# Kernel tuning notes

Measured on AMD Instinct MI355X. Metric: run time of the kernel, lower is better.

## Reference

```python
import jax, jax.numpy as jnp
import numpy as np

L = 32            # fixed label space replacing torch.unique (labels in [0, L))
DELTA_AGG = 0.5
DELTA_DIS = 1.5
REG_W = 0.001


def safe_norm(sq):
    # sqrt with zero-safe gradient: returns 0 where sq == 0
    safe = jnp.where(sq > 0, sq, 1.0)
    return jnp.where(sq > 0, jnp.sqrt(safe), 0.0)


def _single(emb, instance, kernel, training_mask):
    D = emb.shape[0]
    tm = training_mask > 0.5
    kn = kernel > 0.5
    inst = jnp.where(tm, instance, 0).reshape(-1)          # (N,) masked instance labels
    inst_k = jnp.where(tm & kn, instance, 0).reshape(-1)   # (N,) kernel-region labels
    embf = emb.reshape(D, -1).T                            # (N, D)
    ones = jnp.ones(inst.shape, dtype=jnp.float32)

    # per-label kernel means (emb_mean), label 0 stays zero as in torch
    cnt_k = jax.ops.segment_sum(ones, inst_k, num_segments=L)            # (L,)
    sum_k = jax.ops.segment_sum(embf, inst_k, num_segments=L)            # (L, D)
    emb_mean = sum_k / jnp.maximum(cnt_k, 1.0)[:, None]
    emb_mean = emb_mean.at[0].set(0.0)

    present = cnt_k > 0
    num_instance = jnp.sum(present.astype(jnp.int32))
    nz = present & (jnp.arange(L) > 0)

    # aggregation loss: per-pixel distance to own instance's kernel mean
    diff = embf - emb_mean[inst]                                          # (N, D)
    dist = safe_norm(jnp.sum(diff * diff, axis=1))
    val = jnp.log(jax.nn.relu(dist - DELTA_AGG) ** 2 + 1.0)
    sum_v = jax.ops.segment_sum(val, inst, num_segments=L)
    cnt = jax.ops.segment_sum(ones, inst, num_segments=L)
    l_agg_per = sum_v / jnp.maximum(cnt, 1.0)
    l_agg = jnp.sum(jnp.where(nz, l_agg_per, 0.0)) / jnp.maximum(num_instance - 1, 1)

    # discrimination loss: all pairs of distinct non-background present labels
    pdiff = emb_mean[:, None, :] - emb_mean[None, :, :]                   # (L, L, D)
    pdist = safe_norm(jnp.sum(pdiff * pdiff, axis=-1))
    pval = jnp.log(jax.nn.relu(2.0 * DELTA_DIS - pdist) ** 2 + 1.0)
    pmask = nz[:, None] & nz[None, :] & ~jnp.eye(L, dtype=bool)
    n_pairs = jnp.sum(pmask.astype(jnp.float32))
    l_dis = jnp.sum(jnp.where(pmask, pval, 0.0)) / jnp.maximum(n_pairs, 1.0)
    l_dis = jnp.where(num_instance > 2, l_dis, 0.0)

    # regularizer over the num_instance present columns of emb_mean
    reg = jnp.log(safe_norm(jnp.sum(emb_mean * emb_mean, axis=1)) + 1.0)
    l_reg = jnp.sum(jnp.where(present, reg, 0.0)) / jnp.maximum(num_instance, 1) * REG_W

    loss = l_agg + l_dis + l_reg
    return jnp.where(num_instance <= 1, 0.0, loss)


def setup_inputs() -> dict:
    key = jax.random.key(0)
    k1, k2, k3, k4 = jax.random.split(key, 4)
    B, D, H, W = 8, 4, 736, 736
    emb = jax.random.normal(k1, (B, D, H, W), dtype=jnp.float32)
    instance = jax.random.randint(k2, (B, H, W), 0, L, dtype=jnp.int32)
    kernel = jax.random.uniform(k3, (B, H, W), dtype=jnp.float32)
    training_mask = jax.random.uniform(k4, (B, H, W), dtype=jnp.float32)
    return {"emb": emb, "instance": instance, "kernel": kernel, "training_mask": training_mask}


def reference(emb, instance, kernel, training_mask):
    return jax.vmap(_single)(emb, instance, kernel, training_mask)
```

## Files before the change

### kernel.cpp

```cpp
#include <hip/hip_runtime.h>

#define LBL 32
#define NPIX (736 * 736)
#define NQ (NPIX / 4)
#define QPB 512
#define NBA 265
#define BATCH 8
#define DELTA_AGG 0.5f
#define DELTA_DIS 1.5f
#define REG_W 0.001f

#define CE_BASE 0
#define LAB_BASE (BATCH * NPIX * 2)
#define PA_BASE (LAB_BASE + BATCH * NQ)
#define RED_BASE (PA_BASE + BATCH * NBA * 192)
#define PC_BASE (RED_BASE + BATCH * 256)

__device__ __forceinline__ unsigned short f2bf(float f) {
  unsigned int u = __float_as_uint(f);
  unsigned int r = u + 0x7FFFu + ((u >> 16) & 1u);
  return (unsigned short)(r >> 16);
}
__device__ __forceinline__ float bfl(unsigned int w) {
  return __uint_as_float(w << 16);
}
__device__ __forceinline__ float bfh(unsigned int w) {
  return __uint_as_float(w & 0xFFFF0000u);
}

__global__ __launch_bounds__(256) void kA(
    const float* __restrict__ emb, const int* __restrict__ inst,
    const float* __restrict__ kern, const float* __restrict__ mask,
    float* __restrict__ ws) {
  const int b = blockIdx.y;
  const int t = threadIdx.x;
  __shared__ float s_cnt[LBL];
  __shared__ float s_sum[LBL * 4];
  __shared__ float s_cta[LBL];
  if (t < LBL) { s_cnt[t] = 0.f; s_cta[t] = 0.f; }
  if (t < LBL * 4) s_sum[t] = 0.f;
  __syncthreads();

  const long base = (long)b * NPIX;
  const float* ebase = emb + (long)b * 4 * NPIX;
  const int4* ip = (const int4*)(inst + base);
  const float4* kp = (const float4*)(kern + base);
  const float4* mp = (const float4*)(mask + base);
  const float4* p0 = (const float4*)(ebase);
  const float4* p1 = (const float4*)(ebase + NPIX);
  const float4* p2 = (const float4*)(ebase + 2 * NPIX);
  const float4* p3 = (const float4*)(ebase + 3 * NPIX);

  const int q0 = blockIdx.x * QPB + t;
  const int q1 = q0 + 256;
  const bool v1 = (q1 < NQ);

  const int4 iva = ip[q0];
  const float4 kva = kp[q0], mva = mp[q0];
  const float4 ea0 = p0[q0], ea1 = p1[q0], ea2 = p2[q0], ea3 = p3[q0];
  int4 ivb;
  float4 kvb, mvb, fb0, fb1, fb2, fb3;
  if (v1) {
    ivb = ip[q1]; kvb = kp[q1]; mvb = mp[q1];
    fb0 = p0[q1]; fb1 = p1[q1]; fb2 = p2[q1]; fb3 = p3[q1];
  }

  bool has0 = false;
  unsigned int* labp = (unsigned int*)(ws + LAB_BASE) + (size_t)b * NQ;
  uint4* cep = (uint4*)(ws + CE_BASE) + (size_t)b * NQ * 2;

  {
    const int labs[4] = {iva.x, iva.y, iva.z, iva.w};
    const float ks[4] = {kva.x, kva.y, kva.z, kva.w};
    const float ms[4] = {mva.x, mva.y, mva.z, mva.w};
    const float c0[4] = {ea0.x, ea0.y, ea0.z, ea0.w};
    const float c1[4] = {ea1.x, ea1.y, ea1.z, ea1.w};
    const float c2[4] = {ea2.x, ea2.y, ea2.z, ea2.w};
    const float c3[4] = {ea3.x, ea3.y, ea3.z, ea3.w};
    unsigned int labw = 0;
    union { unsigned short us[16]; uint4 v[2]; } pk;
#pragma unroll
    for (int j = 0; j < 4; j++) {
      const bool m = ms[j] > 0.5f;
      const int li = m ? labs[j] : 0;
      const int lk = (m && ks[j] > 0.5f) ? labs[j] : 0;
      labw |= ((unsigned int)li) << (8 * j);
      pk.us[j * 4 + 0] = f2bf(c0[j]);
      pk.us[j * 4 + 1] = f2bf(c1[j]);
      pk.us[j * 4 + 2] = f2bf(c2[j]);
      pk.us[j * 4 + 3] = f2bf(c3[j]);
      if (li > 0) atomicAdd(&s_cta[li], 1.0f);
      if (lk > 0) {
        atomicAdd(&s_cnt[lk], 1.0f);
        atomicAdd(&s_sum[lk * 4 + 0], c0[j]);
        atomicAdd(&s_sum[lk * 4 + 1], c1[j]);
        atomicAdd(&s_sum[lk * 4 + 2], c2[j]);
        atomicAdd(&s_sum[lk * 4 + 3], c3[j]);
      } else {
        has0 = true;
      }
    }
    labp[q0] = labw;
    cep[(size_t)q0 * 2] = pk.v[0];
    cep[(size_t)q0 * 2 + 1] = pk.v[1];
  }
  if (v1) {
    const int labs[4] = {ivb.x, ivb.y, ivb.z, ivb.w};
    const float ks[4] = {kvb.x, kvb.y, kvb.z, kvb.w};
    const float ms[4] = {mvb.x, mvb.y, mvb.z, mvb.w};
    const float c0[4] = {fb0.x, fb0.y, fb0.z, fb0.w};
    const float c1[4] = {fb1.x, fb1.y, fb1.z, fb1.w};
    const float c2[4] = {fb2.x, fb2.y, fb2.z, fb2.w};
    const float c3[4] = {fb3.x, fb3.y, fb3.z, fb3.w};
    unsigned int labw = 0;
    union { unsigned short us[16]; uint4 v[2]; } pk;
#pragma unroll
    for (int j = 0; j < 4; j++) {
      const bool m = ms[j] > 0.5f;
      const int li = m ? labs[j] : 0;
      const int lk = (m && ks[j] > 0.5f) ? labs[j] : 0;
      labw |= ((unsigned int)li) << (8 * j);
      pk.us[j * 4 + 0] = f2bf(c0[j]);
      pk.us[j * 4 + 1] = f2bf(c1[j]);
      pk.us[j * 4 + 2] = f2bf(c2[j]);
      pk.us[j * 4 + 3] = f2bf(c3[j]);
      if (li > 0) atomicAdd(&s_cta[li], 1.0f);
      if (lk > 0) {
        atomicAdd(&s_cnt[lk], 1.0f);
        atomicAdd(&s_sum[lk * 4 + 0], c0[j]);
        atomicAdd(&s_sum[lk * 4 + 1], c1[j]);
        atomicAdd(&s_sum[lk * 4 + 2], c2[j]);
        atomicAdd(&s_sum[lk * 4 + 3], c3[j]);
      } else {
        has0 = true;
      }
    }
    labp[q1] = labw;
    cep[(size_t)q1 * 2] = pk.v[0];
    cep[(size_t)q1 * 2 + 1] = pk.v[1];
  }

  if (has0) s_cnt[0] = 1.0f;
  __syncthreads();
  float* po = ws + PA_BASE + ((size_t)b * NBA + blockIdx.x) * 192;
  if (t < 192)
    po[t] = (t < 32) ? s_cnt[t] : (t < 160 ? s_sum[t - 32] : s_cta[t - 160]);
}

__global__ __launch_bounds__(256) void kB(float* __restrict__ ws) {
  const int b = blockIdx.y;
  const int col = blockIdx.x * 4 + (threadIdx.x >> 6);
  const int lane = threadIdx.x & 63;
  const float* pa = ws + PA_BASE + (size_t)b * NBA * 192 + col;
  float s = 0.f;
  for (int g = lane; g < NBA; g += 64) s += pa[(size_t)g * 192];
#pragma unroll
  for (int o = 32; o > 0; o >>= 1) s += __shfl_down(s, o);
  if (lane == 0) ws[RED_BASE + b * 256 + col] = s;
}

__global__ __launch_bounds__(256) void kC(float* __restrict__ ws) {
  const int b = blockIdx.y;
  const int t = threadIdx.x;
  __shared__ float s_mean[LBL * 4];
  __shared__ float s_val[LBL];
  const float* rd = ws + RED_BASE + b * 256;
  if (t < LBL * 4) {
    const int l = t >> 2;
    s_mean[t] = (l == 0) ? 0.f : rd[32 + t] / fmaxf(rd[l], 1.0f);
  }
  if (t < LBL) s_val[t] = 0.f;
  __syncthreads();

  const unsigned int* labp = (const unsigned int*)(ws + LAB_BASE) + (size_t)b * NQ;
  const uint4* cep = (const uint4*)(ws + CE_BASE) + (size_t)b * NQ * 2;
  const int q0 = blockIdx.x * QPB + t;
  const int q1 = q0 + 256;
  const bool v1 = (q1 < NQ);

  const unsigned int lwa = labp[q0];
  const uint4 ra0 = cep[(size_t)q0 * 2], ra1 = cep[(size_t)q0 * 2 + 1];
  unsigned int lwb = 0;
  uint4 rb0, rb1;
  if (v1) {
    lwb = labp[q1];
    rb0 = cep[(size_t)q1 * 2];
    rb1 = cep[(size_t)q1 * 2 + 1];
  }

  {
    const unsigned int wlo[4] = {ra0.x, ra0.z, ra1.x, ra1.z};
    const unsigned int whi[4] = {ra0.y, ra0.w, ra1.y, ra1.w};
#pragma unroll
    for (int j = 0; j < 4; j++) {
      const int li = (lwa >> (8 * j)) & 0xFF;
      if (li > 0) {
        const float d0 = bfl(wlo[j]) - s_mean[li * 4 + 0];
        const float d1 = bfh(wlo[j]) - s_mean[li * 4 + 1];
        const float d2 = bfl(whi[j]) - s_mean[li * 4 + 2];
        const float d3 = bfh(whi[j]) - s_mean[li * 4 + 3];
        const float sq = d0 * d0 + d1 * d1 + d2 * d2 + d3 * d3;
        const float dist = (sq > 0.f) ? sqrtf(sq) : 0.f;
        const float tt = fmaxf(dist - DELTA_AGG, 0.f);
        atomicAdd(&s_val[li], logf(fmaf(tt, tt, 1.0f)));
      }
    }
  }
  if (v1) {
    const unsigned int wlo[4] = {rb0.x, rb0.z, rb1.x, rb1.z};
    const unsigned int whi[4] = {rb0.y, rb0.w, rb1.y, rb1.w};
#pragma unroll
    for (int j = 0; j < 4; j++) {
      const int li = (lwb >> (8 * j)) & 0xFF;
      if (li > 0) {
        const float d0 = bfl(wlo[j]) - s_mean[li * 4 + 0];
        const float d1 = bfh(wlo[j]) - s_mean[li * 4 + 1];
        const float d2 = bfl(whi[j]) - s_mean[li * 4 + 2];
        const float d3 = bfh(whi[j]) - s_mean[li * 4 + 3];
        const float sq = d0 * d0 + d1 * d1 + d2 * d2 + d3 * d3;
        const float dist = (sq > 0.f) ? sqrtf(sq) : 0.f;
        const float tt = fmaxf(dist - DELTA_AGG, 0.f);
        atomicAdd(&s_val[li], logf(fmaf(tt, tt, 1.0f)));
      }
    }
  }
  __syncthreads();
  float* po = ws + PC_BASE + ((size_t)b * NBA + blockIdx.x) * 32;
  if (t < 32) po[t] = s_val[t];
}

__global__ __launch_bounds__(1024) void kD(const float* __restrict__ ws,
                                           float* __restrict__ out) {
  const int b = blockIdx.x;
  const int t = threadIdx.x;
  const int col = t >> 5, sub = t & 31;
  const float* pc = ws + PC_BASE + (size_t)b * NBA * 32 + col;
  float s = 0.f;
  for (int g = sub; g < NBA; g += 32) s += pc[(size_t)g * 32];
  __shared__ float red[LBL][33];
  red[col][sub] = s;

  const float* rd = ws + RED_BASE + b * 256;
  __shared__ float sm[LBL * 4];
  __shared__ float scc[LBL];
  __shared__ float sca[LBL];
  if (t >= 512 && t < 640) {
    const int e = t - 512, l = e >> 2;
    sm[e] = (l == 0) ? 0.f : rd[32 + e] / fmaxf(rd[l], 1.0f);
  } else if (t >= 640 && t < 672) {
    scc[t - 640] = rd[t - 640];
  } else if (t >= 672 && t < 704) {
    sca[t - 672] = rd[160 + (t - 672)];
  }
  __syncthreads();
  __shared__ float sv[LBL];
  if (t < 32) {
    float v = 0.f;
#pragma unroll
    for (int k = 0; k < 32; k++) v += red[t][k];
    sv[t] = v;
  }
  __syncthreads();

  if (t < 64) {
    const int lane = t;
    const bool pres = (lane < LBL) && (scc[lane & 31] > 0.f);
    const unsigned long long bal_p = __ballot(pres);
    const int num_instance = __popcll(bal_p);
    const bool nz = pres && (lane > 0);
    const unsigned long long bal_nz = __ballot(nz);

    float agg = 0.f;
    if (nz) agg = sv[lane] / fmaxf(sca[lane], 1.0f);

    float reg = 0.f;
    if (pres) {
      float sq = 0.f;
#pragma unroll
      for (int d = 0; d < 4; d++) sq += sm[lane * 4 + d] * sm[lane * 4 + d];
      const float nrm = (sq > 0.f) ? sqrtf(sq) : 0.f;
      reg = logf(nrm + 1.0f);
    }

    float dis = 0.f, npair = 0.f;
    for (int pi = lane; pi < LBL * LBL; pi += 64) {
      const int i = pi >> 5, j = pi & 31;
      if (i != j && ((bal_nz >> i) & 1ull) && ((bal_nz >> j) & 1ull)) {
        float sq = 0.f;
#pragma unroll
        for (int d = 0; d < 4; d++) {
          const float df = sm[i * 4 + d] - sm[j * 4 + d];
          sq += df * df;
        }
        const float pdist = (sq > 0.f) ? sqrtf(sq) : 0.f;
        const float tt = fmaxf(2.0f * DELTA_DIS - pdist, 0.f);
        dis += logf(fmaf(tt, tt, 1.0f));
        npair += 1.0f;
      }
    }

#pragma unroll
    for (int o = 32; o > 0; o >>= 1) {
      agg += __shfl_down(agg, o);
      reg += __shfl_down(reg, o);
      dis += __shfl_down(dis, o);
      npair += __shfl_down(npair, o);
    }

    if (lane == 0) {
      const float l_agg = agg / fmaxf((float)(num_instance - 1), 1.0f);
      const float l_dis = (num_instance > 2) ? dis / fmaxf(npair, 1.0f) : 0.f;
      const float l_reg = reg / fmaxf((float)num_instance, 1.0f) * REG_W;
      const float loss = l_agg + l_dis + l_reg;
      out[b] = (num_instance <= 1) ? 0.f : loss;
    }
  }
}

extern "C" void kernel_launch(void* const* d_in, const int* in_sizes, int n_in,
                              void* d_out, int out_size, void* d_ws,
                              size_t ws_size, hipStream_t stream) {
  const float* emb = (const float*)d_in[0];
  const int* instance = (const int*)d_in[1];
  const float* kern = (const float*)d_in[2];
  const float* mask = (const float*)d_in[3];
  float* out = (float*)d_out;
  float* ws = (float*)d_ws;

  dim3 gridA(NBA, BATCH);
  kA<<<gridA, 256, 0, stream>>>(emb, instance, kern, mask, ws);
  dim3 gridB(48, BATCH);
  kB<<<gridB, 256, 0, stream>>>(ws);
  kC<<<gridA, 256, 0, stream>>>(ws);
  kD<<<BATCH, 1024, 0, stream>>>(ws, out);
}
```

Measured before the change: 182.8 us.

## Drop bf16 embedding copy, reread fp32 emb in kC, wave-aggregate count atomics

Kernel A no longer writes a packed bf16 copy of the embeddings to the workspace. Kernel C now rereads the original fp32 embeddings instead, which removes a 34MB write and the rounding step at the cost of a larger read in kC (68MB instead of 34MB). Kernel A also groups lanes by label through ballots so that count atomics are issued once per label group per wavefront. This adds ballot overhead, while the per-pixel sum atomics stay unchanged. It also makes kC numerically exact, since it now uses fp32 values rather than bf16.

```diff
diff --git a/kernel.cpp b/kernel.cpp
--- a/kernel.cpp
+++ b/kernel.cpp
@@ -10,22 +10,57 @@
 #define DELTA_DIS 1.5f
 #define REG_W 0.001f
 
-#define CE_BASE 0
-#define LAB_BASE (BATCH * NPIX * 2)
-#define PA_BASE (LAB_BASE + BATCH * NQ)
+#define LAB_BASE 0
+#define PA_BASE (BATCH * NQ)
 #define RED_BASE (PA_BASE + BATCH * NBA * 192)
 #define PC_BASE (RED_BASE + BATCH * 256)
 
-__device__ __forceinline__ unsigned short f2bf(float f) {
-  unsigned int u = __float_as_uint(f);
-  unsigned int r = u + 0x7FFFu + ((u >> 16) & 1u);
-  return (unsigned short)(r >> 16);
-}
-__device__ __forceinline__ float bfl(unsigned int w) {
-  return __uint_as_float(w << 16);
-}
-__device__ __forceinline__ float bfh(unsigned int w) {
-  return __uint_as_float(w & 0xFFFF0000u);
+__device__ __forceinline__ unsigned int procQuad(
+    const int4 iv, const float4 kv, const float4 mv,
+    const float4 e0, const float4 e1, const float4 e2, const float4 e3,
+    const int lane, float* __restrict__ s_cnt, float* __restrict__ s_sum,
+    float* __restrict__ s_cta, bool& has0) {
+  const int labs[4] = {iv.x, iv.y, iv.z, iv.w};
+  const float ks[4] = {kv.x, kv.y, kv.z, kv.w};
+  const float ms[4] = {mv.x, mv.y, mv.z, mv.w};
+  const float c0[4] = {e0.x, e0.y, e0.z, e0.w};
+  const float c1[4] = {e1.x, e1.y, e1.z, e1.w};
+  const float c2[4] = {e2.x, e2.y, e2.z, e2.w};
+  const float c3[4] = {e3.x, e3.y, e3.z, e3.w};
+  unsigned int labw = 0;
+#pragma unroll
+  for (int j = 0; j < 4; j++) {
+    const bool m = ms[j] > 0.5f;
+    const int li = m ? labs[j] : 0;
+    const bool kf = m && (ks[j] > 0.5f);
+    labw |= ((unsigned int)li) << (8 * j);
+    const bool act = li > 0;
+    unsigned long long grp = __ballot(act);
+    const unsigned long long kbal = __ballot(act && kf);
+#pragma unroll
+    for (int bb = 0; bb < 5; bb++) {
+      const unsigned long long bal = __ballot((li >> bb) & 1);
+      grp &= ((li >> bb) & 1) ? bal : ~bal;
+    }
+    if (act) {
+      if ((int)__builtin_ctzll(grp) == lane)
+        atomicAdd(&s_cta[li], (float)__popcll(grp));
+      if (kf) {
+        const unsigned long long gk = grp & kbal;
+        if ((int)__builtin_ctzll(gk) == lane)
+          atomicAdd(&s_cnt[li], (float)__popcll(gk));
+        atomicAdd(&s_sum[li * 4 + 0], c0[j]);
+        atomicAdd(&s_sum[li * 4 + 1], c1[j]);
+        atomicAdd(&s_sum[li * 4 + 2], c2[j]);
+        atomicAdd(&s_sum[li * 4 + 3], c3[j]);
+      } else {
+        has0 = true;
+      }
+    } else {
+      has0 = true;
+    }
+  }
+  return labw;
 }
 
 __global__ __launch_bounds__(256) void kA(
@@ -34,6 +69,7 @@
     float* __restrict__ ws) {
   const int b = blockIdx.y;
   const int t = threadIdx.x;
+  const int lane = t & 63;
   __shared__ float s_cnt[LBL];
   __shared__ float s_sum[LBL * 4];
   __shared__ float s_cta[LBL];
@@ -67,77 +103,12 @@
 
   bool has0 = false;
   unsigned int* labp = (unsigned int*)(ws + LAB_BASE) + (size_t)b * NQ;
-  uint4* cep = (uint4*)(ws + CE_BASE) + (size_t)b * NQ * 2;
-
-  {
-    const int labs[4] = {iva.x, iva.y, iva.z, iva.w};
-    const float ks[4] = {kva.x, kva.y, kva.z, kva.w};
-    const float ms[4] = {mva.x, mva.y, mva.z, mva.w};
-    const float c0[4] = {ea0.x, ea0.y, ea0.z, ea0.w};
-    const float c1[4] = {ea1.x, ea1.y, ea1.z, ea1.w};
-    const float c2[4] = {ea2.x, ea2.y, ea2.z, ea2.w};
-    const float c3[4] = {ea3.x, ea3.y, ea3.z, ea3.w};
-    unsigned int labw = 0;
-    union { unsigned short us[16]; uint4 v[2]; } pk;
-#pragma unroll
-    for (int j = 0; j < 4; j++) {
-      const bool m = ms[j] > 0.5f;
-      const int li = m ? labs[j] : 0;
-      const int lk = (m && ks[j] > 0.5f) ? labs[j] : 0;
-      labw |= ((unsigned int)li) << (8 * j);
-      pk.us[j * 4 + 0] = f2bf(c0[j]);
-      pk.us[j * 4 + 1] = f2bf(c1[j]);
-      pk.us[j * 4 + 2] = f2bf(c2[j]);
-      pk.us[j * 4 + 3] = f2bf(c3[j]);
-      if (li > 0) atomicAdd(&s_cta[li], 1.0f);
-      if (lk > 0) {
-        atomicAdd(&s_cnt[lk], 1.0f);
-        atomicAdd(&s_sum[lk * 4 + 0], c0[j]);
-        atomicAdd(&s_sum[lk * 4 + 1], c1[j]);
-        atomicAdd(&s_sum[lk * 4 + 2], c2[j]);
-        atomicAdd(&s_sum[lk * 4 + 3], c3[j]);
-      } else {
-        has0 = true;
-      }
-    }
-    labp[q0] = labw;
-    cep[(size_t)q0 * 2] = pk.v[0];
-    cep[(size_t)q0 * 2 + 1] = pk.v[1];
-  }
+
+  labp[q0] = procQuad(iva, kva, mva, ea0, ea1, ea2, ea3, lane,
+                      s_cnt, s_sum, s_cta, has0);
   if (v1) {
-    const int labs[4] = {ivb.x, ivb.y, ivb.z, ivb.w};
-    const float ks[4] = {kvb.x, kvb.y, kvb.z, kvb.w};
-    const float ms[4] = {mvb.x, mvb.y, mvb.z, mvb.w};
-    const float c0[4] = {fb0.x, fb0.y, fb0.z, fb0.w};
-    const float c1[4] = {fb1.x, fb1.y, fb1.z, fb1.w};
-    const float c2[4] = {fb2.x, fb2.y, fb2.z, fb2.w};
-    const float c3[4] = {fb3.x, fb3.y, fb3.z, fb3.w};
-    unsigned int labw = 0;
-    union { unsigned short us[16]; uint4 v[2]; } pk;
-#pragma unroll
-    for (int j = 0; j < 4; j++) {
-      const bool m = ms[j] > 0.5f;
-      const int li = m ? labs[j] : 0;
-      const int lk = (m && ks[j] > 0.5f) ? labs[j] : 0;
-      labw |= ((unsigned int)li) << (8 * j);
-      pk.us[j * 4 + 0] = f2bf(c0[j]);
-      pk.us[j * 4 + 1] = f2bf(c1[j]);
-      pk.us[j * 4 + 2] = f2bf(c2[j]);
-      pk.us[j * 4 + 3] = f2bf(c3[j]);
-      if (li > 0) atomicAdd(&s_cta[li], 1.0f);
-      if (lk > 0) {
-        atomicAdd(&s_cnt[lk], 1.0f);
-        atomicAdd(&s_sum[lk * 4 + 0], c0[j]);
-        atomicAdd(&s_sum[lk * 4 + 1], c1[j]);
-        atomicAdd(&s_sum[lk * 4 + 2], c2[j]);
-        atomicAdd(&s_sum[lk * 4 + 3], c3[j]);
-      } else {
-        has0 = true;
-      }
-    }
-    labp[q1] = labw;
-    cep[(size_t)q1 * 2] = pk.v[0];
-    cep[(size_t)q1 * 2 + 1] = pk.v[1];
+    labp[q1] = procQuad(ivb, kvb, mvb, fb0, fb1, fb2, fb3, lane,
+                        s_cnt, s_sum, s_cta, has0);
   }
 
   if (has0) s_cnt[0] = 1.0f;
@@ -159,7 +130,31 @@
   if (lane == 0) ws[RED_BASE + b * 256 + col] = s;
 }
 
-__global__ __launch_bounds__(256) void kC(float* __restrict__ ws) {
+__device__ __forceinline__ void aggQuad(const unsigned int lw,
+    const float4 e0, const float4 e1, const float4 e2, const float4 e3,
+    const float* __restrict__ s_mean, float* __restrict__ s_val) {
+  const float c0[4] = {e0.x, e0.y, e0.z, e0.w};
+  const float c1[4] = {e1.x, e1.y, e1.z, e1.w};
+  const float c2[4] = {e2.x, e2.y, e2.z, e2.w};
+  const float c3[4] = {e3.x, e3.y, e3.z, e3.w};
+#pragma unroll
+  for (int j = 0; j < 4; j++) {
+    const int li = (lw >> (8 * j)) & 0xFF;
+    if (li > 0) {
+      const float d0 = c0[j] - s_mean[li * 4 + 0];
+      const float d1 = c1[j] - s_mean[li * 4 + 1];
+      const float d2 = c2[j] - s_mean[li * 4 + 2];
+      const float d3 = c3[j] - s_mean[li * 4 + 3];
+      const float sq = d0 * d0 + d1 * d1 + d2 * d2 + d3 * d3;
+      const float dist = (sq > 0.f) ? sqrtf(sq) : 0.f;
+      const float tt = fmaxf(dist - DELTA_AGG, 0.f);
+      atomicAdd(&s_val[li], logf(fmaf(tt, tt, 1.0f)));
+    }
+  }
+}
+
+__global__ __launch_bounds__(256) void kC(const float* __restrict__ emb,
+                                          float* __restrict__ ws) {
   const int b = blockIdx.y;
   const int t = threadIdx.x;
   __shared__ float s_mean[LBL * 4];
@@ -173,57 +168,27 @@
   __syncthreads();
 
   const unsigned int* labp = (const unsigned int*)(ws + LAB_BASE) + (size_t)b * NQ;
-  const uint4* cep = (const uint4*)(ws + CE_BASE) + (size_t)b * NQ * 2;
+  const float* ebase = emb + (long)b * 4 * NPIX;
+  const float4* p0 = (const float4*)(ebase);
+  const float4* p1 = (const float4*)(ebase + NPIX);
+  const float4* p2 = (const float4*)(ebase + 2 * NPIX);
+  const float4* p3 = (const float4*)(ebase + 3 * NPIX);
   const int q0 = blockIdx.x * QPB + t;
   const int q1 = q0 + 256;
   const bool v1 = (q1 < NQ);
 
   const unsigned int lwa = labp[q0];
-  const uint4 ra0 = cep[(size_t)q0 * 2], ra1 = cep[(size_t)q0 * 2 + 1];
+  const float4 ea0 = p0[q0], ea1 = p1[q0], ea2 = p2[q0], ea3 = p3[q0];
   unsigned int lwb = 0;
-  uint4 rb0, rb1;
+  float4 fb0, fb1, fb2, fb3;
   if (v1) {
     lwb = labp[q1];
-    rb0 = cep[(size_t)q1 * 2];
-    rb1 = cep[(size_t)q1 * 2 + 1];
-  }
-
-  {
-    const unsigned int wlo[4] = {ra0.x, ra0.z, ra1.x, ra1.z};
-    const unsigned int whi[4] = {ra0.y, ra0.w, ra1.y, ra1.w};
-#pragma unroll
-    for (int j = 0; j < 4; j++) {
-      const int li = (lwa >> (8 * j)) & 0xFF;
-      if (li > 0) {
-        const float d0 = bfl(wlo[j]) - s_mean[li * 4 + 0];
-        const float d1 = bfh(wlo[j]) - s_mean[li * 4 + 1];
-        const float d2 = bfl(whi[j]) - s_mean[li * 4 + 2];
-        const float d3 = bfh(whi[j]) - s_mean[li * 4 + 3];
-        const float sq = d0 * d0 + d1 * d1 + d2 * d2 + d3 * d3;
-        const float dist = (sq > 0.f) ? sqrtf(sq) : 0.f;
-        const float tt = fmaxf(dist - DELTA_AGG, 0.f);
-        atomicAdd(&s_val[li], logf(fmaf(tt, tt, 1.0f)));
-      }
-    }
-  }
-  if (v1) {
-    const unsigned int wlo[4] = {rb0.x, rb0.z, rb1.x, rb1.z};
-    const unsigned int whi[4] = {rb0.y, rb0.w, rb1.y, rb1.w};
-#pragma unroll
-    for (int j = 0; j < 4; j++) {
-      const int li = (lwb >> (8 * j)) & 0xFF;
-      if (li > 0) {
-        const float d0 = bfl(wlo[j]) - s_mean[li * 4 + 0];
-        const float d1 = bfh(wlo[j]) - s_mean[li * 4 + 1];
-        const float d2 = bfl(whi[j]) - s_mean[li * 4 + 2];
-        const float d3 = bfh(whi[j]) - s_mean[li * 4 + 3];
-        const float sq = d0 * d0 + d1 * d1 + d2 * d2 + d3 * d3;
-        const float dist = (sq > 0.f) ? sqrtf(sq) : 0.f;
-        const float tt = fmaxf(dist - DELTA_AGG, 0.f);
-        atomicAdd(&s_val[li], logf(fmaf(tt, tt, 1.0f)));
-      }
-    }
-  }
+    fb0 = p0[q1]; fb1 = p1[q1]; fb2 = p2[q1]; fb3 = p3[q1];
+  }
+
+  aggQuad(lwa, ea0, ea1, ea2, ea3, s_mean, s_val);
+  if (v1) aggQuad(lwb, fb0, fb1, fb2, fb3, s_mean, s_val);
+
   __syncthreads();
   float* po = ws + PC_BASE + ((size_t)b * NBA + blockIdx.x) * 32;
   if (t < 32) po[t] = s_val[t];
@@ -331,6 +296,6 @@
   kA<<<gridA, 256, 0, stream>>>(emb, instance, kern, mask, ws);
   dim3 gridB(48, BATCH);
   kB<<<gridB, 256, 0, stream>>>(ws);
-  kC<<<gridA, 256, 0, stream>>>(ws);
+  kC<<<gridA, 256, 0, stream>>>(emb, ws);
   kD<<<BATCH, 1024, 0, stream>>>(ws, out);
 }
```

Measured after the change: 183.5 us. About the same (+0.4%).
